# Optimization experiments

Measured on AMD Instinct MI355X. Metric: run time of the kernel, lower is better.

The kernel has to match this reference:

```python
import jax, jax.numpy as jnp
import numpy as np

NEG_SLOPE = 0.2  # LeakyReLU(0.2) on the final Dense


def setup_inputs() -> dict:
    key = jax.random.key(0)
    k1, k2, k3, k4 = jax.random.split(key, 4)
    B, D = 256, 65536          # batch, input voxel dim
    N, G = 41, 2048            # n_groups, group size (overlapping allowed)
    O, E = 256, 512            # per-group output dim, embed_dim
    x = jax.random.normal(k1, (B, D), dtype=jnp.float32)
    group_idx = jax.random.randint(k2, (N, G), 0, D, dtype=jnp.int32)
    # He-normal-ish init for the per-group Dense weights
    W = jax.random.normal(k3, (N, G, O), dtype=jnp.float32) * np.float32(np.sqrt(2.0 / G))
    b = jnp.zeros((N, O), dtype=jnp.float32)
    W3 = jax.random.normal(k4, (N * O, E), dtype=jnp.float32) * np.float32(np.sqrt(2.0 / (N * O)))
    b3 = jnp.zeros((E,), dtype=jnp.float32)
    return {"x": x, "group_idx": group_idx, "W": W, "b": b, "W3": W3, "b3": b3}


def reference(x, group_idx, W, b, W3, b3):
    B = x.shape[0]
    # per-group gather: (B, N, G)
    g = x[:, group_idx]
    # N parallel Dense layers as one grouped GEMM: (B, N, O)
    h = jnp.einsum('bng,ngo->bno', g, W) + b
    # concat along feature axis -> (B, N*O); dropout is identity at inference
    h = h.reshape(B, -1)
    # final Dense + LeakyReLU(0.2)
    out = h @ W3 + b3
    return jnp.where(out >= 0, out, NEG_SLOPE * out)
```

## Files before the change

### kernel.cpp

```cpp
#include <hip/hip_runtime.h>
#include <hip/hip_bf16.h>

#define NB 256
#define DD 65536
#define NN 41
#define GG 2048
#define OO 256
#define NO 10496
#define EE 512
#define NEG_SLOPE 0.2f

typedef __attribute__((ext_vector_type(8))) short bf16x8;
typedef __attribute__((ext_vector_type(4))) float f32x4;
typedef unsigned int u32;

__device__ __forceinline__ void gl_lds16(const __hip_bfloat16* gsrc, __hip_bfloat16* lds) {
    __builtin_amdgcn_global_load_lds((const __attribute__((address_space(1))) u32*)gsrc,
                                     (__attribute__((address_space(3))) u32*)lds, 16, 0, 0);
}

__device__ __forceinline__ u32 pack_bf2(float lo, float hi) {
    u32 a = (u32)__bfloat16_as_ushort(__float2bfloat16(lo));
    u32 b = (u32)__bfloat16_as_ushort(__float2bfloat16(hi));
    return a | (b << 16);
}

__global__ __launch_bounds__(256) void transpose_both_k(const float* __restrict__ W,
                                                        const float* __restrict__ W3,
                                                        __hip_bfloat16* __restrict__ Wt,
                                                        __hip_bfloat16* __restrict__ W3t) {
    __shared__ u32 tb[64 * 128];
    int bid = blockIdx.x;
    const float* src;
    __hip_bfloat16* dst;
    int K, Oc, kc0, o0;
    if (bid < NN * 32) {
        int z = bid >> 5;
        int rem = bid & 31;
        kc0 = (rem >> 2) * 256;
        o0 = (rem & 3) * 64;
        src = W + (size_t)z * GG * OO;
        dst = Wt + (size_t)z * GG * OO;
        K = GG; Oc = OO;
    } else {
        int rem = bid - NN * 32;
        kc0 = (rem >> 3) * 256;
        o0 = (rem & 7) * 64;
        src = W3; dst = W3t;
        K = NO; Oc = EE;
    }
    int t = threadIdx.x;
    int p = t & 127;
    int oh = (t >> 7) * 32;
    const float* r0 = src + (size_t)(kc0 + 2 * p) * Oc + o0 + oh;
    const float* r1 = r0 + Oc;
#pragma unroll
    for (int c = 0; c < 8; ++c) {
        float4 a = *(const float4*)&r0[c * 4];
        float4 b = *(const float4*)&r1[c * 4];
        tb[(oh + c * 4 + 0) * 128 + p] = pack_bf2(a.x, b.x);
        tb[(oh + c * 4 + 1) * 128 + p] = pack_bf2(a.y, b.y);
        tb[(oh + c * 4 + 2) * 128 + p] = pack_bf2(a.z, b.z);
        tb[(oh + c * 4 + 3) * 128 + p] = pack_bf2(a.w, b.w);
    }
    __syncthreads();
    int w = t >> 6, l = t & 63;
    int lr = l >> 5;
    int ls = l & 31;
#pragma unroll
    for (int j = 0; j < 8; ++j) {
        int o = j * 8 + w * 2 + lr;
        uint4 v = *(const uint4*)&tb[o * 128 + ls * 4];
        *(uint4*)&dst[(size_t)(o0 + o) * K + kc0 + ls * 8] = v;
    }
}

__global__ __launch_bounds__(1024) void gather_full_k(const float* __restrict__ x,
                                                      const int* __restrict__ idx,
                                                      __hip_bfloat16* __restrict__ g) {
    extern __shared__ __hip_bfloat16 xr[];
    int b = blockIdx.x;
    int t = threadIdx.x;
    const float4* xv = (const float4*)(x + (size_t)b * DD);
#pragma unroll
    for (int i = 0; i < 16; ++i) {
        float4 v = xv[t + 1024 * i];
        short4 p;
        p.x = (short)__bfloat16_as_ushort(__float2bfloat16(v.x));
        p.y = (short)__bfloat16_as_ushort(__float2bfloat16(v.y));
        p.z = (short)__bfloat16_as_ushort(__float2bfloat16(v.z));
        p.w = (short)__bfloat16_as_ushort(__float2bfloat16(v.w));
        *(short4*)&xr[(t + 1024 * i) * 4] = p;
    }
    __syncthreads();
    const int4* idx4 = (const int4*)idx;
    for (int u = t; u < NN * GG / 4; u += 1024) {
        int4 ii = idx4[u];
        int n = u >> 9;
        int k = (u & 511) * 4;
        ushort4 o;
        o.x = __bfloat16_as_ushort(xr[ii.x]);
        o.y = __bfloat16_as_ushort(xr[ii.y]);
        o.z = __bfloat16_as_ushort(xr[ii.z]);
        o.w = __bfloat16_as_ushort(xr[ii.w]);
        *(ushort4*)&g[((size_t)n * NB + b) * GG + k] = o;
    }
}

__global__ __launch_bounds__(512) void gather_half_k(const float* __restrict__ x,
                                                     const int* __restrict__ idx,
                                                     __hip_bfloat16* __restrict__ g) {
    __shared__ __align__(16) __hip_bfloat16 xr[32768];
    int b = blockIdx.x >> 1;
    int h = blockIdx.x & 1;
    int t = threadIdx.x;
    const float4* xv = (const float4*)(x + (size_t)b * DD + h * 32768);
#pragma unroll
    for (int i = 0; i < 16; ++i) {
        float4 v = xv[t + 512 * i];
        short4 p;
        p.x = (short)__bfloat16_as_ushort(__float2bfloat16(v.x));
        p.y = (short)__bfloat16_as_ushort(__float2bfloat16(v.y));
        p.z = (short)__bfloat16_as_ushort(__float2bfloat16(v.z));
        p.w = (short)__bfloat16_as_ushort(__float2bfloat16(v.w));
        *(short4*)&xr[(t + 512 * i) * 4] = p;
    }
    __syncthreads();
    const int4* idx4 = (const int4*)idx;
    for (int u = t; u < NN * GG / 4; u += 512) {
        int4 ii = idx4[u];
        int n = u >> 9;
        int k = (u & 511) * 4;
        __hip_bfloat16* dst = &g[((size_t)n * NB + b) * GG + k];
        if ((ii.x >> 15) == h) dst[0] = xr[ii.x & 32767];
        if ((ii.y >> 15) == h) dst[1] = xr[ii.y & 32767];
        if ((ii.z >> 15) == h) dst[2] = xr[ii.z & 32767];
        if ((ii.w >> 15) == h) dst[3] = xr[ii.w & 32767];
    }
}

__global__ __launch_bounds__(256) void gemm1_k(const __hip_bfloat16* __restrict__ g,
                                               const __hip_bfloat16* __restrict__ Wt,
                                               __hip_bfloat16* __restrict__ part1) {
    int bid0 = blockIdx.x;
    int bid = (bid0 & 7) * 82 + (bid0 >> 3);
    int s = bid & 3;
    int o0 = ((bid >> 2) & 1) * 128;
    int m0 = ((bid >> 3) & 1) * 128;
    int n = bid >> 4;
    const __hip_bfloat16* srcA = g + ((size_t)n * NB + m0) * GG + s * 512;
    const __hip_bfloat16* srcB = Wt + ((size_t)n * OO + o0) * GG + s * 512;
    __shared__ __align__(16) __hip_bfloat16 lA[2][128 * 32];
    __shared__ __align__(16) __hip_bfloat16 lB[2][128 * 32];
    int t = threadIdx.x;
    int lane = t & 63, w = t >> 6;
    int mw = (w >> 1) * 64, ow = (w & 1) * 64;
    int lrow = lane & 15, quad = lane >> 4;
    int r0 = t >> 2, q0 = (t & 3) * 8;
    f32x4 acc[4][4] = {};

    gl_lds16(srcA + (size_t)r0 * GG + q0, &lA[0][t * 8]);
    gl_lds16(srcA + (size_t)(r0 + 64) * GG + q0, &lA[0][(t + 256) * 8]);
    gl_lds16(srcB + (size_t)r0 * GG + q0, &lB[0][t * 8]);
    gl_lds16(srcB + (size_t)(r0 + 64) * GG + q0, &lB[0][(t + 256) * 8]);
    __syncthreads();
#pragma unroll 1
    for (int it = 0; it < 16; ++it) {
        int cur = it & 1;
        if (it + 1 < 16) {
            int k1 = (it + 1) * 32;
            gl_lds16(srcA + (size_t)r0 * GG + k1 + q0, &lA[1 - cur][t * 8]);
            gl_lds16(srcA + (size_t)(r0 + 64) * GG + k1 + q0, &lA[1 - cur][(t + 256) * 8]);
            gl_lds16(srcB + (size_t)r0 * GG + k1 + q0, &lB[1 - cur][t * 8]);
            gl_lds16(srcB + (size_t)(r0 + 64) * GG + k1 + q0, &lB[1 - cur][(t + 256) * 8]);
        }
        bf16x8 af[4];
#pragma unroll
        for (int fm = 0; fm < 4; ++fm)
            af[fm] = *(const bf16x8*)&lA[cur][(mw + fm * 16 + lrow) * 32 + quad * 8];
#pragma unroll
        for (int fn = 0; fn < 4; ++fn) {
            bf16x8 bfr = *(const bf16x8*)&lB[cur][(ow + fn * 16 + lrow) * 32 + quad * 8];
#pragma unroll
            for (int fm = 0; fm < 4; ++fm)
                acc[fm][fn] = __builtin_amdgcn_mfma_f32_16x16x32_bf16(af[fm], bfr, acc[fm][fn], 0, 0, 0);
        }
        __syncthreads();
    }
#pragma unroll
    for (int fm = 0; fm < 4; ++fm) {
#pragma unroll
        for (int fn = 0; fn < 4; ++fn) {
            int col = o0 + ow + fn * 16 + lrow;
#pragma unroll
            for (int r = 0; r < 4; ++r) {
                int row = m0 + mw + fm * 16 + quad * 4 + r;
                part1[((size_t)s * NB + row) * NO + n * OO + col] = __float2bfloat16(acc[fm][fn][r]);
            }
        }
    }
}

__global__ __launch_bounds__(256) void combine1_k(const __hip_bfloat16* __restrict__ part1,
                                                  const float* __restrict__ bias,
                                                  __hip_bfloat16* __restrict__ h) {
    int j4 = blockIdx.x * 256 + threadIdx.x;
    int jj = j4 % (NO / 4);
    float4 a = ((const float4*)bias)[jj];
#pragma unroll
    for (int s = 0; s < 4; ++s) {
        ushort4 p = *(const ushort4*)&part1[(size_t)s * NB * NO + (size_t)j4 * 4];
        a.x += __bfloat162float(__ushort_as_bfloat16(p.x));
        a.y += __bfloat162float(__ushort_as_bfloat16(p.y));
        a.z += __bfloat162float(__ushort_as_bfloat16(p.z));
        a.w += __bfloat162float(__ushort_as_bfloat16(p.w));
    }
    ushort4 o;
    o.x = __bfloat16_as_ushort(__float2bfloat16(a.x));
    o.y = __bfloat16_as_ushort(__float2bfloat16(a.y));
    o.z = __bfloat16_as_ushort(__float2bfloat16(a.z));
    o.w = __bfloat16_as_ushort(__float2bfloat16(a.w));
    *(ushort4*)&h[(size_t)j4 * 4] = o;
}

__global__ __launch_bounds__(256) void gemm2_k(const __hip_bfloat16* __restrict__ h,
                                               const __hip_bfloat16* __restrict__ W3t,
                                               float* __restrict__ part) {
    int bid0 = blockIdx.x;
    int bid = (bid0 & 7) * 82 + (bid0 >> 3);
    int e0 = (bid & 7) * 64;
    int m0 = ((bid >> 3) & 1) * 128;
    int s = bid >> 4;
    const __hip_bfloat16* srcA = h + (size_t)m0 * NO + s * 256;
    const __hip_bfloat16* srcB = W3t + (size_t)e0 * NO + s * 256;
    __shared__ __align__(16) __hip_bfloat16 lA[2][128 * 32];
    __shared__ __align__(16) __hip_bfloat16 lB[2][64 * 32];
    int t = threadIdx.x;
    int lane = t & 63, w = t >> 6;
    int mw = (w >> 1) * 64, ew = (w & 1) * 32;
    int lrow = lane & 15, quad = lane >> 4;
    int rA = t >> 2, qA = (t & 3) * 8;
    int rB = t >> 2, qB = (t & 3) * 8;
    f32x4 acc[4][2] = {};

    gl_lds16(srcA + (size_t)rA * NO + qA, &lA[0][t * 8]);
    gl_lds16(srcA + (size_t)(rA + 64) * NO + qA, &lA[0][(t + 256) * 8]);
    gl_lds16(srcB + (size_t)(rB & 63) * NO + qB, &lB[0][t * 8]);
    __syncthreads();
#pragma unroll 1
    for (int it = 0; it < 8; ++it) {
        int cur = it & 1;
        if (it + 1 < 8) {
            int k1 = (it + 1) * 32;
            gl_lds16(srcA + (size_t)rA * NO + k1 + qA, &lA[1 - cur][t * 8]);
            gl_lds16(srcA + (size_t)(rA + 64) * NO + k1 + qA, &lA[1 - cur][(t + 256) * 8]);
            gl_lds16(srcB + (size_t)(rB & 63) * NO + k1 + qB, &lB[1 - cur][t * 8]);
        }
        bf16x8 af[4];
#pragma unroll
        for (int fm = 0; fm < 4; ++fm)
            af[fm] = *(const bf16x8*)&lA[cur][(mw + fm * 16 + lrow) * 32 + quad * 8];
#pragma unroll
        for (int fn = 0; fn < 2; ++fn) {
            bf16x8 bfr = *(const bf16x8*)&lB[cur][(ew + fn * 16 + lrow) * 32 + quad * 8];
#pragma unroll
            for (int fm = 0; fm < 4; ++fm)
                acc[fm][fn] = __builtin_amdgcn_mfma_f32_16x16x32_bf16(af[fm], bfr, acc[fm][fn], 0, 0, 0);
        }
        __syncthreads();
    }
#pragma unroll
    for (int fm = 0; fm < 4; ++fm) {
#pragma unroll
        for (int fn = 0; fn < 2; ++fn) {
            int e = e0 + ew + fn * 16 + lrow;
#pragma unroll
            for (int r = 0; r < 4; ++r) {
                int row = m0 + mw + fm * 16 + quad * 4 + r;
                part[((size_t)s * NB + row) * EE + e] = acc[fm][fn][r];
            }
        }
    }
}

__global__ __launch_bounds__(128) void reduce_k(const float* __restrict__ part,
                                                const float* __restrict__ b3,
                                                float* __restrict__ out) {
    int j = blockIdx.x * 128 + threadIdx.x;
    float4 a = make_float4(0.f, 0.f, 0.f, 0.f);
    for (int s = 0; s < NN; ++s) {
        float4 v = ((const float4*)part)[(size_t)s * (NB * EE / 4) + j];
        a.x += v.x; a.y += v.y; a.z += v.z; a.w += v.w;
    }
    float4 bv = ((const float4*)b3)[j & 127];
    a.x += bv.x; a.y += bv.y; a.z += bv.z; a.w += bv.w;
    a.x = a.x >= 0.f ? a.x : NEG_SLOPE * a.x;
    a.y = a.y >= 0.f ? a.y : NEG_SLOPE * a.y;
    a.z = a.z >= 0.f ? a.z : NEG_SLOPE * a.z;
    a.w = a.w >= 0.f ? a.w : NEG_SLOPE * a.w;
    ((float4*)out)[j] = a;
}

extern "C" void kernel_launch(void* const* d_in, const int* in_sizes, int n_in,
                              void* d_out, int out_size, void* d_ws, size_t ws_size,
                              hipStream_t stream) {
    const float* x = (const float*)d_in[0];
    const int* idx = (const int*)d_in[1];
    const float* W = (const float*)d_in[2];
    const float* bias = (const float*)d_in[3];
    const float* W3 = (const float*)d_in[4];
    const float* b3 = (const float*)d_in[5];
    float* out = (float*)d_out;

    char* ws = (char*)d_ws;
    const size_t g_off = 0;
    const size_t g_sz = (size_t)NN * NB * GG * 2;
    const size_t wt_off = g_off + g_sz;
    const size_t wt_sz = (size_t)NN * GG * OO * 2;
    const size_t w3t_off = wt_off + wt_sz;
    const size_t w3t_sz = (size_t)NO * EE * 2;
    const size_t h_off = w3t_off + w3t_sz;
    const size_t h_sz = (size_t)NB * NO * 2;
    const size_t p_off = h_off + h_sz;

    __hip_bfloat16* g = (__hip_bfloat16*)(ws + g_off);
    __hip_bfloat16* Wt = (__hip_bfloat16*)(ws + wt_off);
    __hip_bfloat16* W3t = (__hip_bfloat16*)(ws + w3t_off);
    __hip_bfloat16* h = (__hip_bfloat16*)(ws + h_off);
    __hip_bfloat16* part1 = (__hip_bfloat16*)(ws + p_off);
    float* part = (float*)(ws + p_off);

    transpose_both_k<<<dim3(NN * 32 + NN * 8), 256, 0, stream>>>(W, W3, Wt, W3t);
    hipError_t aerr = hipFuncSetAttribute(reinterpret_cast<const void*>(gather_full_k),
                                          hipFuncAttributeMaxDynamicSharedMemorySize, 131072);
    if (aerr == hipSuccess) {
        gather_full_k<<<dim3(NB), 1024, 131072, stream>>>(x, idx, g);
    } else {
        gather_half_k<<<dim3(512), 512, 0, stream>>>(x, idx, g);
    }
    gemm1_k<<<dim3(656), 256, 0, stream>>>(g, Wt, part1);
    combine1_k<<<dim3(NB * NO / 4 / 256), 256, 0, stream>>>(part1, bias, h);
    gemm2_k<<<dim3(656), 256, 0, stream>>>(h, W3t, part);
    reduce_k<<<dim3(256), 128, 0, stream>>>(part, b3, out);
}
```

Measured before the change: 276.6 us.

## Fuse W transpose and bf16 conversion into gemm1 B-tile loading

Removes the separate pass that transposed and converted the per-group weights W to bf16. Instead, gemm1 reads fp32 W directly, packs pairs of k-rows into bf16 in registers, and writes them into a swizzled LDS layout, prefetching the next tile into registers while the MFMAs run. This drops a full write and re-read of the transposed weight buffer. In exchange, gemm1 reads twice the bytes for B (fp32 instead of bf16) and does extra conversion work and scattered LDS stores inside the main loop.

```diff
diff --git a/kernel.cpp b/kernel.cpp
--- a/kernel.cpp
+++ b/kernel.cpp
@@ -25,34 +25,17 @@
     return a | (b << 16);
 }
 
-__global__ __launch_bounds__(256) void transpose_both_k(const float* __restrict__ W,
-                                                        const float* __restrict__ W3,
-                                                        __hip_bfloat16* __restrict__ Wt,
-                                                        __hip_bfloat16* __restrict__ W3t) {
+__global__ __launch_bounds__(256) void transpose_w3_k(const float* __restrict__ W3,
+                                                      __hip_bfloat16* __restrict__ W3t) {
     __shared__ u32 tb[64 * 128];
-    int bid = blockIdx.x;
-    const float* src;
-    __hip_bfloat16* dst;
-    int K, Oc, kc0, o0;
-    if (bid < NN * 32) {
-        int z = bid >> 5;
-        int rem = bid & 31;
-        kc0 = (rem >> 2) * 256;
-        o0 = (rem & 3) * 64;
-        src = W + (size_t)z * GG * OO;
-        dst = Wt + (size_t)z * GG * OO;
-        K = GG; Oc = OO;
-    } else {
-        int rem = bid - NN * 32;
-        kc0 = (rem >> 3) * 256;
-        o0 = (rem & 7) * 64;
-        src = W3; dst = W3t;
-        K = NO; Oc = EE;
-    }
+    int rem = blockIdx.x;
+    int kc0 = (rem >> 3) * 256;
+    int o0 = (rem & 7) * 64;
+    const int K = NO, Oc = EE;
     int t = threadIdx.x;
     int p = t & 127;
     int oh = (t >> 7) * 32;
-    const float* r0 = src + (size_t)(kc0 + 2 * p) * Oc + o0 + oh;
+    const float* r0 = W3 + (size_t)(kc0 + 2 * p) * Oc + o0 + oh;
     const float* r1 = r0 + Oc;
 #pragma unroll
     for (int c = 0; c < 8; ++c) {
@@ -71,7 +54,7 @@
     for (int j = 0; j < 8; ++j) {
         int o = j * 8 + w * 2 + lr;
         uint4 v = *(const uint4*)&tb[o * 128 + ls * 4];
-        *(uint4*)&dst[(size_t)(o0 + o) * K + kc0 + ls * 8] = v;
+        *(uint4*)&W3t[(size_t)(o0 + o) * K + kc0 + ls * 8] = v;
     }
 }
 
@@ -140,7 +123,7 @@
 }
 
 __global__ __launch_bounds__(256) void gemm1_k(const __hip_bfloat16* __restrict__ g,
-                                               const __hip_bfloat16* __restrict__ Wt,
+                                               const float* __restrict__ W,
                                                __hip_bfloat16* __restrict__ part1) {
     int bid0 = blockIdx.x;
     int bid = (bid0 & 7) * 82 + (bid0 >> 3);
@@ -149,7 +132,7 @@
     int m0 = ((bid >> 3) & 1) * 128;
     int n = bid >> 4;
     const __hip_bfloat16* srcA = g + ((size_t)n * NB + m0) * GG + s * 512;
-    const __hip_bfloat16* srcB = Wt + ((size_t)n * OO + o0) * GG + s * 512;
+    const float* srcB = W + ((size_t)n * GG + s * 512) * OO + o0;
     __shared__ __align__(16) __hip_bfloat16 lA[2][128 * 32];
     __shared__ __align__(16) __hip_bfloat16 lB[2][128 * 32];
     int t = threadIdx.x;
@@ -157,33 +140,73 @@
     int mw = (w >> 1) * 64, ow = (w & 1) * 64;
     int lrow = lane & 15, quad = lane >> 4;
     int r0 = t >> 2, q0 = (t & 3) * 8;
+    int bp = t >> 4;
+    int boq = t & 15;
+    int bswz = (boq & 3) << 2;
+    const float* wb0 = srcB + (size_t)(2 * bp) * OO + boq * 8;
     f32x4 acc[4][4] = {};
 
+    {
+        float4 a0 = *(const float4*)&wb0[0];
+        float4 a1 = *(const float4*)&wb0[4];
+        float4 b0 = *(const float4*)&wb0[OO];
+        float4 b1 = *(const float4*)&wb0[OO + 4];
+        u32* d = (u32*)&lB[0][0];
+        int ob = boq * 8;
+        int pw = bp ^ bswz;
+        d[(ob + 0) * 16 + pw] = pack_bf2(a0.x, b0.x);
+        d[(ob + 1) * 16 + pw] = pack_bf2(a0.y, b0.y);
+        d[(ob + 2) * 16 + pw] = pack_bf2(a0.z, b0.z);
+        d[(ob + 3) * 16 + pw] = pack_bf2(a0.w, b0.w);
+        d[(ob + 4) * 16 + pw] = pack_bf2(a1.x, b1.x);
+        d[(ob + 5) * 16 + pw] = pack_bf2(a1.y, b1.y);
+        d[(ob + 6) * 16 + pw] = pack_bf2(a1.z, b1.z);
+        d[(ob + 7) * 16 + pw] = pack_bf2(a1.w, b1.w);
+    }
     gl_lds16(srcA + (size_t)r0 * GG + q0, &lA[0][t * 8]);
     gl_lds16(srcA + (size_t)(r0 + 64) * GG + q0, &lA[0][(t + 256) * 8]);
-    gl_lds16(srcB + (size_t)r0 * GG + q0, &lB[0][t * 8]);
-    gl_lds16(srcB + (size_t)(r0 + 64) * GG + q0, &lB[0][(t + 256) * 8]);
     __syncthreads();
 #pragma unroll 1
     for (int it = 0; it < 16; ++it) {
         int cur = it & 1;
-        if (it + 1 < 16) {
+        float4 a0, a1, b0, b1;
+        bool pf = (it + 1 < 16);
+        if (pf) {
             int k1 = (it + 1) * 32;
+            const float* wn = wb0 + (size_t)k1 * OO;
+            a0 = *(const float4*)&wn[0];
+            a1 = *(const float4*)&wn[4];
+            b0 = *(const float4*)&wn[OO];
+            b1 = *(const float4*)&wn[OO + 4];
             gl_lds16(srcA + (size_t)r0 * GG + k1 + q0, &lA[1 - cur][t * 8]);
             gl_lds16(srcA + (size_t)(r0 + 64) * GG + k1 + q0, &lA[1 - cur][(t + 256) * 8]);
-            gl_lds16(srcB + (size_t)r0 * GG + k1 + q0, &lB[1 - cur][t * 8]);
-            gl_lds16(srcB + (size_t)(r0 + 64) * GG + k1 + q0, &lB[1 - cur][(t + 256) * 8]);
         }
         bf16x8 af[4];
 #pragma unroll
         for (int fm = 0; fm < 4; ++fm)
             af[fm] = *(const bf16x8*)&lA[cur][(mw + fm * 16 + lrow) * 32 + quad * 8];
+        const u32* lbu = (const u32*)&lB[cur][0];
 #pragma unroll
         for (int fn = 0; fn < 4; ++fn) {
-            bf16x8 bfr = *(const bf16x8*)&lB[cur][(ow + fn * 16 + lrow) * 32 + quad * 8];
+            int orow = ow + fn * 16 + lrow;
+            int fsw = ((orow >> 3) & 3) << 2;
+            bf16x8 bfr = *(const bf16x8*)&lbu[orow * 16 + (quad * 4 ^ fsw)];
 #pragma unroll
             for (int fm = 0; fm < 4; ++fm)
                 acc[fm][fn] = __builtin_amdgcn_mfma_f32_16x16x32_bf16(af[fm], bfr, acc[fm][fn], 0, 0, 0);
+        }
+        if (pf) {
+            u32* d = (u32*)&lB[1 - cur][0];
+            int ob = boq * 8;
+            int pw = bp ^ bswz;
+            d[(ob + 0) * 16 + pw] = pack_bf2(a0.x, b0.x);
+            d[(ob + 1) * 16 + pw] = pack_bf2(a0.y, b0.y);
+            d[(ob + 2) * 16 + pw] = pack_bf2(a0.z, b0.z);
+            d[(ob + 3) * 16 + pw] = pack_bf2(a0.w, b0.w);
+            d[(ob + 4) * 16 + pw] = pack_bf2(a1.x, b1.x);
+            d[(ob + 5) * 16 + pw] = pack_bf2(a1.y, b1.y);
+            d[(ob + 6) * 16 + pw] = pack_bf2(a1.z, b1.z);
+            d[(ob + 7) * 16 + pw] = pack_bf2(a1.w, b1.w);
         }
         __syncthreads();
     }
@@ -324,13 +347,12 @@
     const size_t p_off = h_off + h_sz;
 
     __hip_bfloat16* g = (__hip_bfloat16*)(ws + g_off);
-    __hip_bfloat16* Wt = (__hip_bfloat16*)(ws + wt_off);
     __hip_bfloat16* W3t = (__hip_bfloat16*)(ws + w3t_off);
     __hip_bfloat16* h = (__hip_bfloat16*)(ws + h_off);
     __hip_bfloat16* part1 = (__hip_bfloat16*)(ws + p_off);
     float* part = (float*)(ws + p_off);
 
-    transpose_both_k<<<dim3(NN * 32 + NN * 8), 256, 0, stream>>>(W, W3, Wt, W3t);
+    transpose_w3_k<<<dim3(NN * 8), 256, 0, stream>>>(W3, W3t);
     hipError_t aerr = hipFuncSetAttribute(reinterpret_cast<const void*>(gather_full_k),
                                           hipFuncAttributeMaxDynamicSharedMemorySize, 131072);
     if (aerr == hipSuccess) {
@@ -338,7 +360,7 @@
     } else {
         gather_half_k<<<dim3(512), 512, 0, stream>>>(x, idx, g);
     }
-    gemm1_k<<<dim3(656), 256, 0, stream>>>(g, Wt, part1);
+    gemm1_k<<<dim3(656), 256, 0, stream>>>(g, W, part1);
     combine1_k<<<dim3(NB * NO / 4 / 256), 256, 0, stream>>>(part1, bias, h);
     gemm2_k<<<dim3(656), 256, 0, stream>>>(h, W3t, part);
     reduce_k<<<dim3(256), 128, 0, stream>>>(part, b3, out);
```

After: 266.2 us. 1.04x faster.
